# Performance work log

Hardware: AMD Instinct MI355X
Metric: run time of the kernel (lower is better)

Reference implementation:

```python
import jax, jax.numpy as jnp
import numpy as np

N = 100000      # nodes
E = 3200000     # edges (avg degree 32)
D = 256         # feature dim
C = 40          # classes
KEEP = 0.5      # 1 - dropout


def setup_inputs() -> dict:
    key = jax.random.key(0)
    k1, k2, k3, k4, k5, k6, k7 = jax.random.split(key, 7)
    x = jax.random.normal(k1, (N, D), dtype=jnp.float32)
    adj_row = jnp.sort(jax.random.randint(k2, (E,), 0, N))
    adj_col = jax.random.randint(k3, (E,), 0, N)
    # roughly degree-normalized edge weights (~1/avg_degree scale)
    adj_vals = jax.random.uniform(k4, (E,), dtype=jnp.float32) * (2.0 / 32.0)
    W = jax.random.normal(k5, (C, D), dtype=jnp.float32) * (1.0 / np.sqrt(D))
    b = jax.random.normal(k6, (C,), dtype=jnp.float32) * 0.01
    # precomputed dropout keep-mask (training mode, p=0.5)
    drop_mask = (jax.random.uniform(k7, (N, D)) < KEEP).astype(jnp.float32)
    return {"x": x, "adj_vals": adj_vals, "W": W, "b": b,
            "drop_mask": drop_mask, "adj_row": adj_row, "adj_col": adj_col}


def reference(x, adj_vals, W, b, drop_mask, adj_row, adj_col):
    n = x.shape[0]

    def spmm(v):  # sparse [N,N] @ dense [N,d] via gather + segment-sum
        return jax.ops.segment_sum(adj_vals[:, None] * v[adj_col], adj_row,
                                   num_segments=n)

    # hidden GraphConvolution (use_linear=False): spmm -> relu -> dropout
    h = jax.nn.relu(spmm(x))
    h = h * drop_mask / KEEP
    # gc_class: Linear(D->C) then spmm
    out = spmm(h @ W.T + b)  # [N, C]
    return out
```

## Files before the change

### kernel.cpp

```cpp
#include <hip/hip_runtime.h>

#define NN 100000
#define EE 3200000
#define DD 256
#define CC 40
#define NCH 16
#define CH 16
#define UN2 8

#define CAP 2432
#define ROWS_PB 64
#define COHORT 192
#define HALFB (COHORT * 8)
#define CHUNK_BLOCKS (2 * HALFB)
#define RG64 1563
#define LROWS 64

__device__ __forceinline__ float bf2f(unsigned int u) {
    return __uint_as_float(u << 16);
}
__device__ __forceinline__ unsigned short f2bf(float f) {
    unsigned int t = __float_as_uint(f);
    return (unsigned short)((t + 0x7FFFu + ((t >> 16) & 1u)) >> 16);
}

__global__ __launch_bounds__(256) void k_row_ptr(const int* __restrict__ adj_row,
                                                 int* __restrict__ row_ptr) {
    int e = blockIdx.x * 256 + threadIdx.x;
    if (e >= EE) return;
    int r = adj_row[e];
    int prev = (e == 0) ? -1 : adj_row[e - 1];
    for (int rr = prev + 1; rr <= r; ++rr) row_ptr[rr] = e;
    if (e == EE - 1) {
        for (int rr = r + 1; rr <= NN; ++rr) row_ptr[rr] = EE;
    }
}

__global__ __launch_bounds__(256) void k_cvt_t(const float* __restrict__ x,
                                               ushort* __restrict__ xb) {
    __shared__ ushort ls[32][DD + 4];
    int t = threadIdx.x;
    size_t r0 = (size_t)blockIdx.x * 32;
    const float4* src = (const float4*)(x + r0 * DD);
#pragma unroll
    for (int u = 0; u < 8; ++u) {
        int idx = u * 256 + t;
        float4 v = src[idx];
        int row = idx >> 6, d4 = idx & 63;
        ushort* p = &ls[row][d4 * 4];
        p[0] = f2bf(v.x); p[1] = f2bf(v.y); p[2] = f2bf(v.z); p[3] = f2bf(v.w);
    }
    __syncthreads();
    int c = t >> 4, rp = t & 15;
    const uint4* s0 = (const uint4*)&ls[2 * rp][c * CH];
    const uint4* s1 = (const uint4*)&ls[2 * rp + 1][c * CH];
    uint4* dst = (uint4*)(xb + ((size_t)c * NN + r0 + 2 * rp) * CH);
    dst[0] = s0[0];
    dst[1] = s0[1];
    dst[2] = s1[0];
    dst[3] = s1[1];
}

__global__ __launch_bounds__(256, 8) void k_chunk(
    const ushort* __restrict__ xb, const float* __restrict__ adj_vals,
    const int* __restrict__ adj_col, const int* __restrict__ row_ptr,
    const float* __restrict__ drop_mask, ushort* __restrict__ hb)
{
    __shared__ uint2 meta[CAP + 8];
    int bid = blockIdx.x;
    int half = (bid >= HALFB) ? 1 : 0;
    int rem = bid - half * HALFB;
    int c = (rem & 7) + half * 8;
    int q = rem >> 3;
    int wave = threadIdx.x >> 6, lane = threadIdx.x & 63;
    int g = lane >> 2, i = lane & 3;
    const ushort* xc = xb + (size_t)c * NN * CH;

    for (int rg = q; rg < RG64; rg += COHORT) {
        int row0 = rg * ROWS_PB;
        int row  = row0 + wave * 16 + g;
        bool rv  = row < NN;
        int rend = min(row0 + ROWS_PB, NN);
        int e_start = __builtin_amdgcn_readfirstlane(row_ptr[row0]);
        int e_end   = __builtin_amdgcn_readfirstlane(row_ptr[rend]);
        int nstage  = min(e_end - e_start, CAP);

        for (int t = threadIdx.x; t < nstage; t += 256) {
            uint2 m;
            m.x = (unsigned)adj_col[e_start + t];
            m.y = __float_as_uint(adj_vals[e_start + t]);
            meta[t] = m;
        }
        __syncthreads();

        int e0  = rv ? row_ptr[row] : 0;
        int cnt = rv ? row_ptr[row + 1] - e0 : 0;
        int eloc = e0 - e_start;
        float a0 = 0.f, a1 = 0.f, a2 = 0.f, a3 = 0.f;

        if (eloc + cnt <= nstage) {
            int body = cnt & ~(UN2 - 1);
            int k = 0;
            for (; k < body; k += UN2) {
                uint2 mm[UN2];
#pragma unroll
                for (int u = 0; u < UN2; ++u) mm[u] = meta[eloc + k + u];
                uint2 xv[UN2];
#pragma unroll
                for (int u = 0; u < UN2; ++u)
                    xv[u] = *(const uint2*)(xc + (size_t)mm[u].x * CH + i * 4);
#pragma unroll
                for (int u = 0; u < UN2; ++u) {
                    float v = __uint_as_float(mm[u].y);
                    a0 = fmaf(v, bf2f(xv[u].x & 0xFFFFu), a0);
                    a1 = fmaf(v, bf2f(xv[u].x >> 16),     a1);
                    a2 = fmaf(v, bf2f(xv[u].y & 0xFFFFu), a2);
                    a3 = fmaf(v, bf2f(xv[u].y >> 16),     a3);
                }
            }
            if (k < cnt) {
#pragma unroll
                for (int u = 0; u < UN2; ++u) {
                    int kk = k + u;
                    uint2 m = meta[eloc + min(kk, cnt - 1)];
                    float v = (kk < cnt) ? __uint_as_float(m.y) : 0.f;
                    uint2 xv = *(const uint2*)(xc + (size_t)m.x * CH + i * 4);
                    a0 = fmaf(v, bf2f(xv.x & 0xFFFFu), a0);
                    a1 = fmaf(v, bf2f(xv.x >> 16),     a1);
                    a2 = fmaf(v, bf2f(xv.y & 0xFFFFu), a2);
                    a3 = fmaf(v, bf2f(xv.y >> 16),     a3);
                }
            }
        } else {
            for (int k = 0; k < cnt; ++k) {
                int idx = e0 + k;
                float v = adj_vals[idx];
                int col = adj_col[idx];
                uint2 xv = *(const uint2*)(xc + (size_t)col * CH + i * 4);
                a0 = fmaf(v, bf2f(xv.x & 0xFFFFu), a0);
                a1 = fmaf(v, bf2f(xv.x >> 16),     a1);
                a2 = fmaf(v, bf2f(xv.y & 0xFFFFu), a2);
                a3 = fmaf(v, bf2f(xv.y >> 16),     a3);
            }
        }
        __syncthreads();

        if (rv) {
            size_t off = (size_t)row * DD + c * CH + i * 4;
            const float* mp = drop_mask + off;
            float m0 = __builtin_nontemporal_load(mp);
            float m1 = __builtin_nontemporal_load(mp + 1);
            float m2 = __builtin_nontemporal_load(mp + 2);
            float m3 = __builtin_nontemporal_load(mp + 3);
            float h0 = fmaxf(a0, 0.f) * m0 * 2.f;
            float h1 = fmaxf(a1, 0.f) * m1 * 2.f;
            float h2 = fmaxf(a2, 0.f) * m2 * 2.f;
            float h3 = fmaxf(a3, 0.f) * m3 * 2.f;
            unsigned long long pk =
                (unsigned long long)((unsigned)f2bf(h0) | ((unsigned)f2bf(h1) << 16)) |
                ((unsigned long long)((unsigned)f2bf(h2) | ((unsigned)f2bf(h3) << 16)) << 32);
            __builtin_nontemporal_store(pk, (unsigned long long*)(hb + off));
        }
    }
}

__global__ __launch_bounds__(256) void k_linear(
    const ushort* __restrict__ hb, const float* __restrict__ W,
    const float* __restrict__ b, float* __restrict__ z)
{
    __shared__ float ws[CC][DD + 4];
    int t = threadIdx.x;
    for (int idx = t; idx < CC * (DD / 4); idx += 256) {
        int c = idx >> 6, k4 = idx & 63;
        float4 v = ((const float4*)(W + (size_t)c * DD))[k4];
        float* p = &ws[c][k4 * 4];
        p[0] = v.x; p[1] = v.y; p[2] = v.z; p[3] = v.w;
    }
    __syncthreads();

    int row = blockIdx.x * LROWS + (t >> 2);
    int cg = (t & 3) * 10;
    if (row >= NN) return;

    const uint4* hrow = (const uint4*)(hb + (size_t)row * DD);
    float acc[10] = {0.f, 0.f, 0.f, 0.f, 0.f, 0.f, 0.f, 0.f, 0.f, 0.f};

    for (int k8 = 0; k8 < DD / 8; ++k8) {
        uint4 hv = hrow[k8];
        float h0 = bf2f(hv.x & 0xFFFFu), h1 = bf2f(hv.x >> 16);
        float h2 = bf2f(hv.y & 0xFFFFu), h3 = bf2f(hv.y >> 16);
        float h4 = bf2f(hv.z & 0xFFFFu), h5 = bf2f(hv.z >> 16);
        float h6 = bf2f(hv.w & 0xFFFFu), h7 = bf2f(hv.w >> 16);
#pragma unroll
        for (int j = 0; j < 10; ++j) {
            const float* wp = &ws[cg + j][k8 * 8];
            float4 wa = *(const float4*)wp;
            float4 wb = *(const float4*)(wp + 4);
            acc[j] = fmaf(h0, wa.x, fmaf(h1, wa.y,
                     fmaf(h2, wa.z, fmaf(h3, wa.w, acc[j]))));
            acc[j] = fmaf(h4, wb.x, fmaf(h5, wb.y,
                     fmaf(h6, wb.z, fmaf(h7, wb.w, acc[j]))));
        }
    }
#pragma unroll
    for (int j = 0; j < 10; ++j)
        z[(size_t)row * CC + cg + j] = acc[j] + b[cg + j];
}

__global__ __launch_bounds__(256) void k_spmm2(
    const float* __restrict__ z, const float* __restrict__ adj_vals,
    const int* __restrict__ adj_col, const int* __restrict__ row_ptr,
    float* __restrict__ out)
{
    int wave = threadIdx.x >> 6;
    int lane = threadIdx.x & 63;
    int row = blockIdx.x * 4 + wave;
    int cl = lane < CC ? lane : CC - 1;

    int e0 = __builtin_amdgcn_readfirstlane(row_ptr[row]);
    int e1 = __builtin_amdgcn_readfirstlane(row_ptr[row + 1]);

    float acc = 0.f;
    int nb = (e1 - e0 + UN2 - 1) / UN2;
    for (int bI = 0; bI < nb; ++bI) {
        int base = e0 + bI * UN2;
        float vv[UN2]; int cc[UN2];
#pragma unroll
        for (int u = 0; u < UN2; ++u) {
            int idx = base + u;
            bool ok = idx < e1;
            idx = ok ? idx : e1 - 1;
            vv[u] = ok ? adj_vals[idx] : 0.f;
            cc[u] = adj_col[idx];
        }
        float za[UN2];
#pragma unroll
        for (int u = 0; u < UN2; ++u)
            za[u] = z[(size_t)cc[u] * CC + cl];
#pragma unroll
        for (int u = 0; u < UN2; ++u)
            acc = fmaf(vv[u], za[u], acc);
    }
    if (lane < CC) out[(size_t)row * CC + lane] = acc;
}

extern "C" void kernel_launch(void* const* d_in, const int* in_sizes, int n_in,
                              void* d_out, int out_size, void* d_ws, size_t ws_size,
                              hipStream_t stream) {
    const float* x         = (const float*)d_in[0];
    const float* adj_vals  = (const float*)d_in[1];
    const float* W         = (const float*)d_in[2];
    const float* b         = (const float*)d_in[3];
    const float* drop_mask = (const float*)d_in[4];
    const int*   adj_row   = (const int*)d_in[5];
    const int*   adj_col   = (const int*)d_in[6];
    float* out = (float*)d_out;

    char* wsp = (char*)d_ws;
    size_t rp_bytes = ((size_t)(NN + 1) * 4 + 255) & ~(size_t)255;
    size_t z_bytes  = (size_t)NN * CC * 4;
    size_t xb_bytes = (size_t)NN * DD * 2;
    int* row_ptr = (int*)wsp;
    float* zbuf  = (float*)(wsp + rp_bytes);
    ushort* xb   = (ushort*)(wsp + rp_bytes + z_bytes);
    ushort* hb   = (ushort*)(wsp + rp_bytes + z_bytes + xb_bytes);

    hipLaunchKernelGGL(k_row_ptr, dim3((EE + 255) / 256), dim3(256), 0, stream,
                       adj_row, row_ptr);
    hipLaunchKernelGGL(k_cvt_t, dim3(NN / 32), dim3(256), 0, stream, x, xb);
    hipLaunchKernelGGL(k_chunk, dim3(CHUNK_BLOCKS), dim3(256), 0, stream,
                       xb, adj_vals, adj_col, row_ptr, drop_mask, hb);
    hipLaunchKernelGGL(k_linear, dim3((NN + LROWS - 1) / LROWS), dim3(256), 0,
                       stream, hb, W, b, zbuf);
    hipLaunchKernelGGL(k_spmm2, dim3(NN / 4), dim3(256), 0, stream,
                       zbuf, adj_vals, adj_col, row_ptr, out);
}
```

Before: 551.6 us.

## Widen feature chunks to 32 bf16 columns with 16-byte gathers per lane

Changes the chunked bf16 feature layout from 16 chunks of 16 columns to 8 chunks of 32 columns, so each lane gathers 16 bytes (8 features) per edge instead of 8. This halves how often the edge metadata is staged and walked per chunk and makes each gather wider. The cost is more accumulator registers, which lowers the occupancy bound from 8 to 7 blocks, and a larger footprint per chunk that may hurt cache residency. The block-to-chunk mapping and grid size are adjusted to match.

```diff
diff --git a/kernel.cpp b/kernel.cpp
--- a/kernel.cpp
+++ b/kernel.cpp
@@ -4,15 +4,14 @@
 #define EE 3200000
 #define DD 256
 #define CC 40
-#define NCH 16
-#define CH 16
+#define NCH 8
+#define CH 32
 #define UN2 8
 
 #define CAP 2432
 #define ROWS_PB 64
-#define COHORT 192
-#define HALFB (COHORT * 8)
-#define CHUNK_BLOCKS (2 * HALFB)
+#define COHORT 256
+#define CHUNK_BLOCKS (COHORT * 8)
 #define RG64 1563
 #define LROWS 64
 
@@ -51,27 +50,24 @@
         p[0] = f2bf(v.x); p[1] = f2bf(v.y); p[2] = f2bf(v.z); p[3] = f2bf(v.w);
     }
     __syncthreads();
-    int c = t >> 4, rp = t & 15;
-    const uint4* s0 = (const uint4*)&ls[2 * rp][c * CH];
-    const uint4* s1 = (const uint4*)&ls[2 * rp + 1][c * CH];
-    uint4* dst = (uint4*)(xb + ((size_t)c * NN + r0 + 2 * rp) * CH);
-    dst[0] = s0[0];
-    dst[1] = s0[1];
-    dst[2] = s1[0];
-    dst[3] = s1[1];
-}
-
-__global__ __launch_bounds__(256, 8) void k_chunk(
+    int c = t >> 5, r = t & 31;
+    const uint4* s = (const uint4*)&ls[r][c * CH];
+    uint4* dst = (uint4*)(xb + ((size_t)c * NN + r0 + r) * CH);
+    dst[0] = s[0];
+    dst[1] = s[1];
+    dst[2] = s[2];
+    dst[3] = s[3];
+}
+
+__global__ __launch_bounds__(256, 7) void k_chunk(
     const ushort* __restrict__ xb, const float* __restrict__ adj_vals,
     const int* __restrict__ adj_col, const int* __restrict__ row_ptr,
     const float* __restrict__ drop_mask, ushort* __restrict__ hb)
 {
     __shared__ uint2 meta[CAP + 8];
     int bid = blockIdx.x;
-    int half = (bid >= HALFB) ? 1 : 0;
-    int rem = bid - half * HALFB;
-    int c = (rem & 7) + half * 8;
-    int q = rem >> 3;
+    int c = bid & 7;
+    int q = bid >> 3;
     int wave = threadIdx.x >> 6, lane = threadIdx.x & 63;
     int g = lane >> 2, i = lane & 3;
     const ushort* xc = xb + (size_t)c * NN * CH;
@@ -97,6 +93,7 @@
         int cnt = rv ? row_ptr[row + 1] - e0 : 0;
         int eloc = e0 - e_start;
         float a0 = 0.f, a1 = 0.f, a2 = 0.f, a3 = 0.f;
+        float a4 = 0.f, a5 = 0.f, a6 = 0.f, a7 = 0.f;
 
         if (eloc + cnt <= nstage) {
             int body = cnt & ~(UN2 - 1);
@@ -105,10 +102,10 @@
                 uint2 mm[UN2];
 #pragma unroll
                 for (int u = 0; u < UN2; ++u) mm[u] = meta[eloc + k + u];
-                uint2 xv[UN2];
+                uint4 xv[UN2];
 #pragma unroll
                 for (int u = 0; u < UN2; ++u)
-                    xv[u] = *(const uint2*)(xc + (size_t)mm[u].x * CH + i * 4);
+                    xv[u] = *(const uint4*)(xc + (size_t)mm[u].x * CH + i * 8);
 #pragma unroll
                 for (int u = 0; u < UN2; ++u) {
                     float v = __uint_as_float(mm[u].y);
@@ -116,6 +113,10 @@
                     a1 = fmaf(v, bf2f(xv[u].x >> 16),     a1);
                     a2 = fmaf(v, bf2f(xv[u].y & 0xFFFFu), a2);
                     a3 = fmaf(v, bf2f(xv[u].y >> 16),     a3);
+                    a4 = fmaf(v, bf2f(xv[u].z & 0xFFFFu), a4);
+                    a5 = fmaf(v, bf2f(xv[u].z >> 16),     a5);
+                    a6 = fmaf(v, bf2f(xv[u].w & 0xFFFFu), a6);
+                    a7 = fmaf(v, bf2f(xv[u].w >> 16),     a7);
                 }
             }
             if (k < cnt) {
@@ -124,11 +125,15 @@
                     int kk = k + u;
                     uint2 m = meta[eloc + min(kk, cnt - 1)];
                     float v = (kk < cnt) ? __uint_as_float(m.y) : 0.f;
-                    uint2 xv = *(const uint2*)(xc + (size_t)m.x * CH + i * 4);
+                    uint4 xv = *(const uint4*)(xc + (size_t)m.x * CH + i * 8);
                     a0 = fmaf(v, bf2f(xv.x & 0xFFFFu), a0);
                     a1 = fmaf(v, bf2f(xv.x >> 16),     a1);
                     a2 = fmaf(v, bf2f(xv.y & 0xFFFFu), a2);
                     a3 = fmaf(v, bf2f(xv.y >> 16),     a3);
+                    a4 = fmaf(v, bf2f(xv.z & 0xFFFFu), a4);
+                    a5 = fmaf(v, bf2f(xv.z >> 16),     a5);
+                    a6 = fmaf(v, bf2f(xv.w & 0xFFFFu), a6);
+                    a7 = fmaf(v, bf2f(xv.w >> 16),     a7);
                 }
             }
         } else {
@@ -136,30 +141,46 @@
                 int idx = e0 + k;
                 float v = adj_vals[idx];
                 int col = adj_col[idx];
-                uint2 xv = *(const uint2*)(xc + (size_t)col * CH + i * 4);
+                uint4 xv = *(const uint4*)(xc + (size_t)col * CH + i * 8);
                 a0 = fmaf(v, bf2f(xv.x & 0xFFFFu), a0);
                 a1 = fmaf(v, bf2f(xv.x >> 16),     a1);
                 a2 = fmaf(v, bf2f(xv.y & 0xFFFFu), a2);
                 a3 = fmaf(v, bf2f(xv.y >> 16),     a3);
+                a4 = fmaf(v, bf2f(xv.z & 0xFFFFu), a4);
+                a5 = fmaf(v, bf2f(xv.z >> 16),     a5);
+                a6 = fmaf(v, bf2f(xv.w & 0xFFFFu), a6);
+                a7 = fmaf(v, bf2f(xv.w >> 16),     a7);
             }
         }
         __syncthreads();
 
         if (rv) {
-            size_t off = (size_t)row * DD + c * CH + i * 4;
+            size_t off = (size_t)row * DD + c * CH + i * 8;
             const float* mp = drop_mask + off;
             float m0 = __builtin_nontemporal_load(mp);
             float m1 = __builtin_nontemporal_load(mp + 1);
             float m2 = __builtin_nontemporal_load(mp + 2);
             float m3 = __builtin_nontemporal_load(mp + 3);
+            float m4 = __builtin_nontemporal_load(mp + 4);
+            float m5 = __builtin_nontemporal_load(mp + 5);
+            float m6 = __builtin_nontemporal_load(mp + 6);
+            float m7 = __builtin_nontemporal_load(mp + 7);
             float h0 = fmaxf(a0, 0.f) * m0 * 2.f;
             float h1 = fmaxf(a1, 0.f) * m1 * 2.f;
             float h2 = fmaxf(a2, 0.f) * m2 * 2.f;
             float h3 = fmaxf(a3, 0.f) * m3 * 2.f;
-            unsigned long long pk =
+            float h4 = fmaxf(a4, 0.f) * m4 * 2.f;
+            float h5 = fmaxf(a5, 0.f) * m5 * 2.f;
+            float h6 = fmaxf(a6, 0.f) * m6 * 2.f;
+            float h7 = fmaxf(a7, 0.f) * m7 * 2.f;
+            unsigned long long p0 =
                 (unsigned long long)((unsigned)f2bf(h0) | ((unsigned)f2bf(h1) << 16)) |
                 ((unsigned long long)((unsigned)f2bf(h2) | ((unsigned)f2bf(h3) << 16)) << 32);
-            __builtin_nontemporal_store(pk, (unsigned long long*)(hb + off));
+            unsigned long long p1 =
+                (unsigned long long)((unsigned)f2bf(h4) | ((unsigned)f2bf(h5) << 16)) |
+                ((unsigned long long)((unsigned)f2bf(h6) | ((unsigned)f2bf(h7) << 16)) << 32);
+            __builtin_nontemporal_store(p0, (unsigned long long*)(hb + off));
+            __builtin_nontemporal_store(p1, (unsigned long long*)(hb + off + 4));
         }
     }
 }
```

After: 465.9 us. 1.18x faster.
